# Optimization experiments

Hardware: AMD Instinct MI355X
Metric: run time of the kernel (lower is better)

Reference implementation:

```python
import math
import jax, jax.numpy as jnp
import numpy as np

B, L, D_MODEL = 2, 2048, 1024
N_HEAD, HEAD_DIM = 16, 64
ATT_SCALE = 1.0  # divisor is sqrt(head_dim ** attention_scale)


def setup_inputs() -> dict:
    key = jax.random.key(0)
    ks = jax.random.split(key, 6)
    HD = N_HEAD * HEAD_DIM
    # Xavier-uniform style init for projection weights (stored as [in, out])
    def xavier(k, fan_in, fan_out):
        lim = math.sqrt(6.0 / (fan_in + fan_out))
        return jax.random.uniform(k, (fan_in, fan_out), jnp.float32, -lim, lim)
    return {
        "x":  jax.random.normal(ks[0], (B, L, D_MODEL), jnp.float32),
        "Wq": xavier(ks[1], D_MODEL, HD), "bq": jnp.zeros((HD,), jnp.float32),
        "Wk": xavier(ks[2], D_MODEL, HD), "bk": jnp.zeros((HD,), jnp.float32),
        "Wv": xavier(ks[3], D_MODEL, HD), "bv": jnp.zeros((HD,), jnp.float32),
        "Wo": xavier(ks[4], HD, D_MODEL),
        "bo": jax.random.uniform(ks[5], (D_MODEL,), jnp.float32, -1.0 / math.sqrt(HD), 1.0 / math.sqrt(HD)),
    }


def reference(x, Wq, bq, Wk, bk, Wv, bv, Wo, bo):
    b, l, _ = x.shape
    # QKV projections -> [B, L, H, Dh]
    q = (x @ Wq + bq).reshape(b, l, N_HEAD, HEAD_DIM)
    k = (x @ Wk + bk).reshape(b, l, N_HEAD, HEAD_DIM)
    v = (x @ Wv + bv).reshape(b, l, N_HEAD, HEAD_DIM)
    scale = 1.0 / math.sqrt(HEAD_DIM ** ATT_SCALE)
    # Unnormalized (no softmax) attention: (Q K^T / sqrt(Dh)) V
    scores = jnp.einsum("blhd,bmhd->bhlm", q, k) * scale  # [B,H,L,L]
    attn = jnp.einsum("bhlm,bmhd->blhd", scores, v)        # [B,L,H,Dh]
    out = attn.reshape(b, l, N_HEAD * HEAD_DIM) @ Wo + bo  # dispatcher
    return out
```

## Files before the change

kernel.cpp:

```cpp
#include <hip/hip_runtime.h>
#include <stdint.h>

#define B_ 2
#define L_ 2048
#define DM 1024
#define NH 16
#define DH 64
#define M_ (B_*L_)

typedef short short8 __attribute__((ext_vector_type(8)));
typedef float f32x4 __attribute__((ext_vector_type(4)));

__device__ __forceinline__ unsigned short f2b(float f) {
    union { float f; unsigned int u; } v; v.f = f;
    unsigned int u = v.u;
    return (unsigned short)((u + 0x7fffu + ((u >> 16) & 1u)) >> 16);
}

__device__ __forceinline__ void gld_lds16(const void* g, void* l) {
    __builtin_amdgcn_global_load_lds(
        (const __attribute__((address_space(1))) void*)g,
        (__attribute__((address_space(3))) void*)l, 16, 0, 0);
}

__global__ __launch_bounds__(256)
void setup_kernel(const float* __restrict__ x,
                  const float* __restrict__ Wq, const float* __restrict__ Wk,
                  const float* __restrict__ Wv, const float* __restrict__ Wo,
                  const float* __restrict__ bq, const float* __restrict__ bk,
                  const float* __restrict__ bv,
                  unsigned short* __restrict__ xb, unsigned short* __restrict__ WqkvT,
                  unsigned short* __restrict__ WoT, float* __restrict__ biasq,
                  float* __restrict__ KtV)
{
    __shared__ float tile[32][33];
    const int bid = blockIdx.x;
    const int t = threadIdx.x;

    if (bid < 2048) {
        int i = (bid * 256 + t) * 8;
        float4 a0 = *(const float4*)(x + i);
        float4 a1 = *(const float4*)(x + i + 4);
        uint4 p;
        p.x = (unsigned)f2b(a0.x) | ((unsigned)f2b(a0.y) << 16);
        p.y = (unsigned)f2b(a0.z) | ((unsigned)f2b(a0.w) << 16);
        p.z = (unsigned)f2b(a1.x) | ((unsigned)f2b(a1.y) << 16);
        p.w = (unsigned)f2b(a1.z) | ((unsigned)f2b(a1.w) << 16);
        *(uint4*)(xb + i) = p;
    } else if (bid < 2048 + 4096) {
        int wb = bid - 2048;
        int wi = wb >> 10;
        int tid = wb & 1023;
        const float* W = (wi == 0) ? Wq : (wi == 1) ? Wk : (wi == 2) ? Wv : Wo;
        float s = (wi == 1) ? 0.125f : 1.0f;
        int n0 = (tid & 31) * 32, k0 = (tid >> 5) * 32;
        int r = t >> 3, c4 = (t & 7) << 2;
        float4 v = *(const float4*)(W + (size_t)(k0 + r) * DM + n0 + c4);
        tile[r][c4+0] = v.x; tile[r][c4+1] = v.y; tile[r][c4+2] = v.z; tile[r][c4+3] = v.w;
        __syncthreads();
        uint2 o;
        o.x = (unsigned)f2b(tile[c4+0][r]*s) | ((unsigned)f2b(tile[c4+1][r]*s) << 16);
        o.y = (unsigned)f2b(tile[c4+2][r]*s) | ((unsigned)f2b(tile[c4+3][r]*s) << 16);
        int f = n0 + r;
        size_t drow;
        unsigned short* dst;
        if (wi == 0)      { dst = WqkvT; drow = f; }
        else if (wi == 1) { dst = WqkvT; drow = 1024 + (f >> 6) * 128 + (f & 63); }
        else if (wi == 2) { dst = WqkvT; drow = 1024 + (f >> 6) * 128 + 64 + (f & 63); }
        else              { dst = WoT;   drow = f; }
        *(uint2*)(dst + drow * DM + k0 + c4) = o;
    } else if (bid < 2048 + 4096 + 12) {
        int n = (bid - 6144) * 256 + t;
        float v;
        if (n < 1024) v = bq[n];
        else {
            int kv = (n - 1024) >> 7, r = (n - 1024) & 127;
            v = (r < 64) ? 0.125f * bk[kv * 64 + r] : bv[kv * 64 + (r - 64)];
        }
        biasq[n] = v;
    } else {
        int i = ((bid - 6156) * 256 + t) * 4;
        float4 z; z.x = z.y = z.z = z.w = 0.f;
        *(float4*)(KtV + i) = z;
    }
}

__global__ __launch_bounds__(512, 2)
void qkv_fused_kernel(const unsigned short* __restrict__ A,
                      const unsigned short* __restrict__ Bt,
                      const float* __restrict__ biasq,
                      unsigned short* __restrict__ Qb,
                      float* __restrict__ KtV)
{
    __shared__ __align__(16) char smem[131072];

    const int bid = blockIdx.x;
    const int mt = bid & 15;
    const int nt = bid >> 4;
    const int m0 = mt * 256, n0 = nt * 256;

    const int t = threadIdx.x;
    const int w = t >> 6, lane = t & 63;
    const int quad = lane >> 4, l16 = lane & 15;
    const int wr = w >> 2, wc = w & 3;

    f32x4 acc[8][4];
    #pragma unroll
    for (int i = 0; i < 8; i++)
        #pragma unroll
        for (int j = 0; j < 4; j++)
            #pragma unroll
            for (int r = 0; r < 4; r++) acc[i][j][r] = 0.f;

    const int c0 = t, c1 = 512 + t;
    const int row0 = c0 >> 2, g0 = (c0 & 3) ^ ((row0 >> 1) & 3);
    const int row1 = c1 >> 2, g1 = (c1 & 3) ^ ((row1 >> 1) & 3);

    auto STAGE_A = [&](int buf, int kk) {
        gld_lds16(A + (size_t)(m0 + row0) * DM + kk + g0 * 8,
                  smem + buf * 32768 + w * 1024);
        gld_lds16(A + (size_t)(m0 + row1) * DM + kk + g1 * 8,
                  smem + buf * 32768 + 8192 + w * 1024);
    };
    auto STAGE_B = [&](int buf, int kk) {
        gld_lds16(Bt + (size_t)(n0 + row0) * DM + kk + g0 * 8,
                  smem + buf * 32768 + 16384 + w * 1024);
        gld_lds16(Bt + (size_t)(n0 + row1) * DM + kk + g1 * 8,
                  smem + buf * 32768 + 16384 + 8192 + w * 1024);
    };

    STAGE_A(0, 0);  STAGE_B(0, 0);
    STAGE_A(1, 32); STAGE_B(1, 32);

    int cur = 0, st = 2;
    short8 bf[4], af[4];

    for (int T = 0; T < 31; T++) {
        asm volatile("s_waitcnt vmcnt(4)" ::: "memory");
        __builtin_amdgcn_sched_barrier(0);
        __builtin_amdgcn_s_barrier();
        __builtin_amdgcn_sched_barrier(0);

        const char* Ab = smem + cur * 32768;
        const char* Bb = Ab + 16384;

        if (T < 30) STAGE_A(st, (T + 2) * 32);
        #pragma unroll
        for (int j = 0; j < 4; j++) {
            int bn = wc * 64 + j * 16 + l16;
            bf[j] = *(const short8*)(Bb + bn * 64 + ((quad ^ ((bn >> 1) & 3)) << 4));
        }
        #pragma unroll
        for (int i = 0; i < 4; i++) {
            int am = wr * 128 + i * 16 + l16;
            af[i] = *(const short8*)(Ab + am * 64 + ((quad ^ ((am >> 1) & 3)) << 4));
        }
        __builtin_amdgcn_s_setprio(1);
        #pragma unroll
        for (int i = 0; i < 4; i++)
            #pragma unroll
            for (int j = 0; j < 4; j++)
                acc[i][j] = __builtin_amdgcn_mfma_f32_16x16x32_bf16(af[i], bf[j], acc[i][j], 0, 0, 0);
        __builtin_amdgcn_s_setprio(0);

        if (T < 30) STAGE_B(st, (T + 2) * 32);
        #pragma unroll
        for (int i = 0; i < 4; i++) {
            int am = wr * 128 + (i + 4) * 16 + l16;
            af[i] = *(const short8*)(Ab + am * 64 + ((quad ^ ((am >> 1) & 3)) << 4));
        }
        __builtin_amdgcn_s_setprio(1);
        #pragma unroll
        for (int i = 0; i < 4; i++)
            #pragma unroll
            for (int j = 0; j < 4; j++)
                acc[i + 4][j] = __builtin_amdgcn_mfma_f32_16x16x32_bf16(af[i], bf[j], acc[i + 4][j], 0, 0, 0);
        __builtin_amdgcn_s_setprio(0);

        cur = (cur == 2) ? 0 : cur + 1;
        st  = (st  == 2) ? 0 : st  + 1;
    }

    asm volatile("s_waitcnt vmcnt(0)" ::: "memory");
    __builtin_amdgcn_sched_barrier(0);
    __builtin_amdgcn_s_barrier();
    __builtin_amdgcn_sched_barrier(0);
    {
        const char* Ab = smem + cur * 32768;
        const char* Bb = Ab + 16384;
        #pragma unroll
        for (int j = 0; j < 4; j++) {
            int bn = wc * 64 + j * 16 + l16;
            bf[j] = *(const short8*)(Bb + bn * 64 + ((quad ^ ((bn >> 1) & 3)) << 4));
        }
        #pragma unroll
        for (int i = 0; i < 4; i++) {
            int am = wr * 128 + i * 16 + l16;
            af[i] = *(const short8*)(Ab + am * 64 + ((quad ^ ((am >> 1) & 3)) << 4));
        }
        #pragma unroll
        for (int i = 0; i < 4; i++)
            #pragma unroll
            for (int j = 0; j < 4; j++)
                acc[i][j] = __builtin_amdgcn_mfma_f32_16x16x32_bf16(af[i], bf[j], acc[i][j], 0, 0, 0);
        #pragma unroll
        for (int i = 0; i < 4; i++) {
            int am = wr * 128 + (i + 4) * 16 + l16;
            af[i] = *(const short8*)(Ab + am * 64 + ((quad ^ ((am >> 1) & 3)) << 4));
        }
        #pragma unroll
        for (int i = 0; i < 4; i++)
            #pragma unroll
            for (int j = 0; j < 4; j++)
                acc[i + 4][j] = __builtin_amdgcn_mfma_f32_16x16x32_bf16(af[i], bf[j], acc[i + 4][j], 0, 0, 0);
    }

    #pragma unroll
    for (int j = 0; j < 4; j++) {
        float bv = biasq[n0 + wc * 64 + j * 16 + l16];
        #pragma unroll
        for (int i = 0; i < 8; i++)
            #pragma unroll
            for (int r = 0; r < 4; r++) acc[i][j][r] += bv;
    }

    if (nt < 4) {
        #pragma unroll
        for (int j = 0; j < 4; j++) {
            int col = n0 + wc * 64 + j * 16 + l16;
            #pragma unroll
            for (int i = 0; i < 8; i++) {
                #pragma unroll
                for (int r = 0; r < 4; r++) {
                    int row = m0 + wr * 128 + i * 16 + quad * 4 + r;
                    Qb[(size_t)row * DM + col] = f2b(acc[i][j][r]);
                }
            }
        }
        return;
    }

    __builtin_amdgcn_sched_barrier(0);
    __builtin_amdgcn_s_barrier();

    #pragma unroll
    for (int j = 0; j < 4; j++) {
        int c = wc * 64 + j * 16 + l16;
        int cs = (c & 7) << 4;
        #pragma unroll
        for (int i = 0; i < 8; i++) {
            int l0 = wr * 128 + i * 16 + quad * 4;
            uint2 o;
            o.x = (unsigned)f2b(acc[i][j][0]) | ((unsigned)f2b(acc[i][j][1]) << 16);
            o.y = (unsigned)f2b(acc[i][j][2]) | ((unsigned)f2b(acc[i][j][3]) << 16);
            *(uint2*)(smem + c * 512 + ((l0 * 2) ^ cs)) = o;
        }
    }
    __builtin_amdgcn_sched_barrier(0);
    __builtin_amdgcn_s_barrier();

    const int hh = w >> 2;
    const int s  = w & 3;
    const int bb = mt >> 3;
    const int h  = (nt - 4) * 2 + hh;

    f32x4 kacc[4];
    #pragma unroll
    for (int j = 0; j < 4; j++)
        #pragma unroll
        for (int r = 0; r < 4; r++) kacc[j][r] = 0.f;

    #pragma unroll
    for (int ks = 0; ks < 8; ks++) {
        int ca = hh * 128 + s * 16 + l16;
        short8 afk = *(const short8*)(smem + ca * 512 + ((ks * 64 + quad * 16) ^ ((ca & 7) << 4)));
        #pragma unroll
        for (int j = 0; j < 4; j++) {
            int cb = hh * 128 + 64 + j * 16 + l16;
            short8 bfk = *(const short8*)(smem + cb * 512 + ((ks * 64 + quad * 16) ^ ((cb & 7) << 4)));
            kacc[j] = __builtin_amdgcn_mfma_f32_16x16x32_bf16(afk, bfk, kacc[j], 0, 0, 0);
        }
    }

    float* dst = KtV + (size_t)(bb * NH + h) * 64 * 64;
    #pragma unroll
    for (int j = 0; j < 4; j++) {
        int col = j * 16 + l16;
        #pragma unroll
        for (int r = 0; r < 4; r++) {
            int row = s * 16 + quad * 4 + r;
            atomicAdd(dst + row * 64 + col, kacc[j][r]);
        }
    }
}

__global__ __launch_bounds__(256)
void zmat_kernel(const unsigned short* __restrict__ WoT, const float* __restrict__ KtV,
                 unsigned short* __restrict__ ZT)
{
    __shared__ __align__(16) unsigned short Asl[64][72];
    __shared__ __align__(16) unsigned short Bsl[64][72];

    const int bh = blockIdx.x, nt0 = blockIdx.y;
    const int b = bh >> 4, h = bh & 15;
    const int t = threadIdx.x;
    const int wave = t >> 6, lane = t & 63;
    const int quad = lane >> 4, l16 = lane & 15;
    const int n0 = nt0 * 64;
    const int row = t >> 2, c0 = (t & 3) << 4;

    const unsigned short* ap = WoT + (size_t)(n0 + row) * DM + h * DH + c0;
    *(uint4*)&Asl[row][c0]     = *(const uint4*)ap;
    *(uint4*)&Asl[row][c0 + 8] = *(const uint4*)(ap + 8);

    const float* kp = KtV + ((size_t)bh * 64 + row) * 64 + c0;
    #pragma unroll
    for (int j = 0; j < 16; j++) Bsl[row][c0 + j] = f2b(kp[j]);
    __syncthreads();

    f32x4 acc[4];
    #pragma unroll
    for (int i = 0; i < 4; i++)
        #pragma unroll
        for (int r = 0; r < 4; r++) acc[i][r] = 0.f;

    #pragma unroll
    for (int ks = 0; ks < 2; ks++) {
        short8 af = *(const short8*)&Asl[wave * 16 + l16][ks * 32 + quad * 8];
        #pragma unroll
        for (int nt = 0; nt < 4; nt++) {
            short8 bfr = *(const short8*)&Bsl[nt * 16 + l16][ks * 32 + quad * 8];
            acc[nt] = __builtin_amdgcn_mfma_f32_16x16x32_bf16(af, bfr, acc[nt], 0, 0, 0);
        }
    }

    unsigned short* zb = ZT + (size_t)b * 1024 * 1024 + (size_t)h * DH;
    #pragma unroll
    for (int nt = 0; nt < 4; nt++) {
        int col = nt * 16 + l16;
        #pragma unroll
        for (int r = 0; r < 4; r++) {
            int zr = n0 + wave * 16 + quad * 4 + r;
            zb[(size_t)zr * 1024 + col] = f2b(acc[nt][r]);
        }
    }
}

__global__ __launch_bounds__(256)
void out_gemm_kernel(const unsigned short* __restrict__ A,
                     const unsigned short* __restrict__ Bt,
                     const float* __restrict__ bias,
                     float* __restrict__ C)
{
    __shared__ __align__(16) unsigned short As[128 * 64];
    __shared__ __align__(16) unsigned short Bs[64 * 64];

    const int bid = blockIdx.x;
    const int xcd = bid & 7, local = bid >> 3;
    const int mt = xcd * 4 + (local & 3);
    const int nt = local >> 2;
    const int m0 = mt * 128, n0 = nt * 64;

    const int t = threadIdx.x;
    const int w = t >> 6, lane = t & 63;
    const int quad = lane >> 4, l16 = lane & 15;

    const unsigned short* Btb = Bt + (size_t)(m0 >> 11) * 1024 * 1024;

    f32x4 acc[2][4];
    #pragma unroll
    for (int i = 0; i < 2; i++)
        #pragma unroll
        for (int j = 0; j < 4; j++)
            #pragma unroll
            for (int r = 0; r < 4; r++) acc[i][j][r] = 0.f;

    for (int kk = 0; kk < DM; kk += 64) {
        #pragma unroll
        for (int p = 0; p < 4; p++) {
            int c = p * 256 + t;
            int row = c >> 3, slot = c & 7;
            int g = slot ^ ((row >> 1) & 7);
            gld_lds16(A + (size_t)(m0 + row) * DM + kk + g * 8,
                      (char*)As + p * 4096 + w * 1024);
        }
        #pragma unroll
        for (int p = 0; p < 2; p++) {
            int c = p * 256 + t;
            int row = c >> 3, slot = c & 7;
            int g = slot ^ ((row >> 1) & 7);
            gld_lds16(Btb + (size_t)(n0 + row) * DM + kk + g * 8,
                      (char*)Bs + p * 4096 + w * 1024);
        }
        __syncthreads();

        #pragma unroll
        for (int ks = 0; ks < 2; ks++) {
            int kc = ks * 4 + quad;
            short8 afr[2], bfr[4];
            #pragma unroll
            for (int i = 0; i < 2; i++) {
                int am = w * 32 + i * 16 + l16;
                afr[i] = *(const short8*)((const char*)As + am * 128 + ((kc ^ ((am >> 1) & 7)) << 4));
            }
            #pragma unroll
            for (int j = 0; j < 4; j++) {
                int bn = j * 16 + l16;
                bfr[j] = *(const short8*)((const char*)Bs + bn * 128 + ((kc ^ ((bn >> 1) & 7)) << 4));
            }
            #pragma unroll
            for (int i = 0; i < 2; i++)
                #pragma unroll
                for (int j = 0; j < 4; j++)
                    acc[i][j] = __builtin_amdgcn_mfma_f32_16x16x32_bf16(afr[i], bfr[j], acc[i][j], 0, 0, 0);
        }
        __syncthreads();
    }

    #pragma unroll
    for (int j = 0; j < 4; j++) {
        int col = n0 + j * 16 + l16;
        float bv = bias[col];
        #pragma unroll
        for (int i = 0; i < 2; i++) {
            #pragma unroll
            for (int r = 0; r < 4; r++) {
                int row = m0 + w * 32 + i * 16 + quad * 4 + r;
                C[(size_t)row * DM + col] = acc[i][j][r] + bv;
            }
        }
    }
}


extern "C" void kernel_launch(void* const* d_in, const int* in_sizes, int n_in,
                              void* d_out, int out_size, void* d_ws, size_t ws_size,
                              hipStream_t stream)
{
    const float* x  = (const float*)d_in[0];
    const float* Wq = (const float*)d_in[1];
    const float* bq = (const float*)d_in[2];
    const float* Wk = (const float*)d_in[3];
    const float* bk = (const float*)d_in[4];
    const float* Wv = (const float*)d_in[5];
    const float* bv = (const float*)d_in[6];
    const float* Wo = (const float*)d_in[7];
    const float* bo = (const float*)d_in[8];

    char* ws = (char*)d_ws;
    unsigned short* xb    = (unsigned short*)(ws);
    unsigned short* WqkvT = (unsigned short*)(ws + (size_t)8  * 1024 * 1024);
    unsigned short* WoT   = (unsigned short*)(ws + (size_t)14 * 1024 * 1024);
    float*          biasq = (float*)         (ws + (size_t)16 * 1024 * 1024);
    unsigned short* Qb    = (unsigned short*)(ws + (size_t)17 * 1024 * 1024);
    unsigned short* ZT    = (unsigned short*)(ws + (size_t)25 * 1024 * 1024);
    float*          KtV   = (float*)         (ws + (size_t)29 * 1024 * 1024);

    setup_kernel<<<6284, 256, 0, stream>>>(x, Wq, Wk, Wv, Wo, bq, bk, bv,
                                           xb, WqkvT, WoT, biasq, KtV);

    qkv_fused_kernel<<<192, 512, 0, stream>>>(xb, WqkvT, biasq, Qb, KtV);

    zmat_kernel<<<dim3(B_ * NH, 16), 256, 0, stream>>>(WoT, KtV, ZT);

    out_gemm_kernel<<<512, 256, 0, stream>>>(Qb, ZT, bo, (float*)d_out);
}
```

Measured before the change: 142.2 us.

## Triple-buffer output GEMM LDS staging with async loads and MFMA priority

The output projection GEMM gets a three-stage LDS ring buffer. Global-to-LDS loads for tiles k+2 are issued while the MFMAs for tile k run, with vmcnt-based waits and a single barrier per iteration in place of two syncthreads. MFMA sections are also wrapped in s_setprio to favour the math waves. This is meant to hide global load latency in the K loop, at the cost of 72 KB LDS per block, which can reduce occupancy.

Measured after the change: 138.3 us, median of 2. -2.8%, faster.

```diff
diff --git a/kernel.cpp b/kernel.cpp
--- a/kernel.cpp
+++ b/kernel.cpp
@@ -352,8 +352,7 @@
                      const float* __restrict__ bias,
                      float* __restrict__ C)
 {
-    __shared__ __align__(16) unsigned short As[128 * 64];
-    __shared__ __align__(16) unsigned short Bs[64 * 64];
+    __shared__ __align__(16) char smem[73728];
 
     const int bid = blockIdx.x;
     const int xcd = bid & 7, local = bid >> 3;
@@ -375,14 +374,14 @@
             #pragma unroll
             for (int r = 0; r < 4; r++) acc[i][j][r] = 0.f;
 
-    for (int kk = 0; kk < DM; kk += 64) {
+    auto STAGE = [&](int buf, int kk) {
         #pragma unroll
         for (int p = 0; p < 4; p++) {
             int c = p * 256 + t;
             int row = c >> 3, slot = c & 7;
             int g = slot ^ ((row >> 1) & 7);
             gld_lds16(A + (size_t)(m0 + row) * DM + kk + g * 8,
-                      (char*)As + p * 4096 + w * 1024);
+                      smem + buf * 24576 + p * 4096 + w * 1024);
         }
         #pragma unroll
         for (int p = 0; p < 2; p++) {
@@ -390,10 +389,12 @@
             int row = c >> 3, slot = c & 7;
             int g = slot ^ ((row >> 1) & 7);
             gld_lds16(Btb + (size_t)(n0 + row) * DM + kk + g * 8,
-                      (char*)Bs + p * 4096 + w * 1024);
-        }
-        __syncthreads();
-
+                      smem + buf * 24576 + 16384 + p * 4096 + w * 1024);
+        }
+    };
+    auto COMPUTE = [&](int buf) {
+        const char* Asb = smem + buf * 24576;
+        const char* Bsb = Asb + 16384;
         #pragma unroll
         for (int ks = 0; ks < 2; ks++) {
             int kc = ks * 4 + quad;
@@ -401,21 +402,44 @@
             #pragma unroll
             for (int i = 0; i < 2; i++) {
                 int am = w * 32 + i * 16 + l16;
-                afr[i] = *(const short8*)((const char*)As + am * 128 + ((kc ^ ((am >> 1) & 7)) << 4));
+                afr[i] = *(const short8*)(Asb + am * 128 + ((kc ^ ((am >> 1) & 7)) << 4));
             }
             #pragma unroll
             for (int j = 0; j < 4; j++) {
                 int bn = j * 16 + l16;
-                bfr[j] = *(const short8*)((const char*)Bs + bn * 128 + ((kc ^ ((bn >> 1) & 7)) << 4));
+                bfr[j] = *(const short8*)(Bsb + bn * 128 + ((kc ^ ((bn >> 1) & 7)) << 4));
             }
+            __builtin_amdgcn_s_setprio(1);
             #pragma unroll
             for (int i = 0; i < 2; i++)
                 #pragma unroll
                 for (int j = 0; j < 4; j++)
                     acc[i][j] = __builtin_amdgcn_mfma_f32_16x16x32_bf16(afr[i], bfr[j], acc[i][j], 0, 0, 0);
-        }
-        __syncthreads();
-    }
+            __builtin_amdgcn_s_setprio(0);
+        }
+    };
+
+    STAGE(0, 0);
+    STAGE(1, 64);
+
+    int cur = 0, st = 2;
+    for (int T = 0; T < 15; T++) {
+        asm volatile("s_waitcnt vmcnt(6)" ::: "memory");
+        __builtin_amdgcn_sched_barrier(0);
+        __builtin_amdgcn_s_barrier();
+        __builtin_amdgcn_sched_barrier(0);
+
+        if (T < 14) STAGE(st, (T + 2) * 64);
+        COMPUTE(cur);
+
+        cur = (cur == 2) ? 0 : cur + 1;
+        st  = (st  == 2) ? 0 : st  + 1;
+    }
+    asm volatile("s_waitcnt vmcnt(0)" ::: "memory");
+    __builtin_amdgcn_sched_barrier(0);
+    __builtin_amdgcn_s_barrier();
+    __builtin_amdgcn_sched_barrier(0);
+    COMPUTE(cur);
 
     #pragma unroll
     for (int j = 0; j < 4; j++) {
```
